# Kernel tuning notes

Hardware: AMD Instinct MI355X
Metric: run time of the kernel (lower is better)

## Reference

```python
import jax, jax.numpy as jnp
import numpy as np

DIM, NH, NS = 384, 8, 3
HID = int(DIM * 4.0)
R1 = max(1, int(min(DIM, HID) * 0.5))   # 192
R2 = max(1, int(min(HID, DIM) * 0.5))   # 192
SPLIT = DIM // NS                        # 128
HD = DIM // NH                           # 48


def _ln(x, g, b, eps=1e-6):
    m = jnp.mean(x, axis=-1, keepdims=True)
    v = jnp.mean(jnp.square(x - m), axis=-1, keepdims=True)
    return (x - m) * jax.lax.rsqrt(v + eps) * g + b


def _dwconv(x, w, b):
    # x: [B, SPLIT, H, W]; w: [SPLIT, 1, 3, 3] depthwise (groups=SPLIT)
    y = jax.lax.conv_general_dilated(
        x, w, window_strides=(1, 1), padding='SAME',
        dimension_numbers=('NCHW', 'OIHW', 'NCHW'),
        feature_group_count=SPLIT)
    return y + b[None, :, None, None]


def setup_inputs() -> dict:
    key = jax.random.key(0)
    ks = jax.random.split(key, 16)
    s = lambda *sh: 0.02
    inp = {
        'x': jax.random.normal(ks[0], (16, DIM, 56, 56), jnp.float32),
        'dw_w0': jax.random.normal(ks[1], (SPLIT, 1, 3, 3), jnp.float32) * 0.1,
        'dw_b0': jnp.zeros((SPLIT,), jnp.float32),
        'dw_w1': jax.random.normal(ks[2], (SPLIT, 1, 3, 3), jnp.float32) * 0.1,
        'dw_b1': jnp.zeros((SPLIT,), jnp.float32),
        'ln1_g': jnp.ones((DIM,), jnp.float32),
        'ln1_b': jnp.zeros((DIM,), jnp.float32),
        'qkv_w': jax.random.normal(ks[3], (DIM, 3 * DIM), jnp.float32) * 0.02,
        'proj_w': jax.random.normal(ks[4], (DIM, DIM), jnp.float32) * 0.02,
        'proj_b': jnp.zeros((DIM,), jnp.float32),
        'ln2_g': jnp.ones((DIM,), jnp.float32),
        'ln2_b': jnp.zeros((DIM,), jnp.float32),
        'mlp1_dw': jax.random.normal(ks[5], (DIM, R1), jnp.float32) * 0.02,
        'mlp1_uw': jax.random.normal(ks[6], (R1, HID), jnp.float32) * 0.02,
        'mlp1_ub': jnp.zeros((HID,), jnp.float32),
        'mlp2_dw': jax.random.normal(ks[7], (HID, R2), jnp.float32) * 0.02,
        'mlp2_uw': jax.random.normal(ks[8], (R2, DIM), jnp.float32) * 0.02,
        'mlp2_ub': jnp.zeros((DIM,), jnp.float32),
    }
    return inp


def reference(x, dw_w0, dw_b0, dw_w1, dw_b1, ln1_g, ln1_b, qkv_w,
              proj_w, proj_b, ln2_g, ln2_b,
              mlp1_dw, mlp1_uw, mlp1_ub, mlp2_dw, mlp2_uw, mlp2_ub):
    B, C, H, W = x.shape
    # multi-scale depthwise residual chain
    s0, s1, s2 = jnp.split(x, NS, axis=1)
    s1 = _dwconv(s1 + s0, dw_w0, dw_b0)
    s2 = _dwconv(s2 + s1, dw_w1, dw_b1)
    x = jnp.concatenate([s0, s1, s2], axis=1)

    N = H * W
    x_flat = jnp.transpose(x.reshape(B, C, N), (0, 2, 1))  # [B, N, C]
    y = _ln(x_flat, ln1_g, ln1_b)
    qkv = (y @ qkv_w).reshape(B, N, 3, NH, HD)
    q = jnp.transpose(qkv[:, :, 0], (0, 2, 3, 1))  # [B, NH, HD, N]
    k = jnp.transpose(qkv[:, :, 1], (0, 2, 3, 1))
    v = jnp.transpose(qkv[:, :, 2], (0, 2, 3, 1))
    # L2 normalize over token dim (XCA)
    q = q / jnp.maximum(jnp.linalg.norm(q, axis=-1, keepdims=True), 1e-12)
    k = k / jnp.maximum(jnp.linalg.norm(k, axis=-1, keepdims=True), 1e-12)
    attn = jnp.einsum('bhdn,bhen->bhde', q, k)  # [B, NH, HD, HD]
    attn = jax.nn.softmax(attn, axis=-1)
    y = jnp.einsum('bhde,bhen->bhdn', attn, v)  # [B, NH, HD, N]
    y = jnp.transpose(y, (0, 3, 1, 2)).reshape(B, N, C)
    y = y @ proj_w + proj_b
    x_flat = x_flat + y

    z = _ln(x_flat, ln2_g, ln2_b)
    h = jax.nn.gelu((z @ mlp1_dw) @ mlp1_uw + mlp1_ub, approximate=False)
    z = (h @ mlp2_dw) @ mlp2_uw + mlp2_ub
    x_flat = x_flat + z
    return jnp.transpose(x_flat, (0, 2, 1)).reshape(B, C, H, W)
```

## Files before the change

kernel.cpp:

```cpp
#include <hip/hip_runtime.h>


typedef __attribute__((ext_vector_type(8))) short short8;
typedef __attribute__((ext_vector_type(4))) float floatx4;

#define NB 16
#define DIM 384
#define NTOK 3136
#define TTOK 50176
#define NH 8
#define HD 48

__device__ __forceinline__ unsigned short f2bf(float f) {
  union { float f; unsigned int u; } v; v.f = f;
  unsigned int u = v.u;
  unsigned int r = (u + 0x7FFFu + ((u >> 16) & 1u)) >> 16;
  return (unsigned short)r;
}
__device__ __forceinline__ float bf2f(unsigned short h) {
  union { unsigned int u; float f; } v; v.u = ((unsigned int)h) << 16;
  return v.f;
}

__device__ __forceinline__ void gload_lds16(const unsigned short* g, unsigned short* l) {
  __builtin_amdgcn_global_load_lds(
      (const __attribute__((address_space(1))) unsigned int*)g,
      (__attribute__((address_space(3))) unsigned int*)l, 16, 0, 0);
}

__global__ void wtrans(const float* __restrict__ w, unsigned short* __restrict__ wt,
                       int K, int N) {
  int g = blockIdx.x * 256 + threadIdx.x;
  if (g < K * N) {
    int k = g / N, n = g % N;
    wt[(size_t)n * K + k] = f2bf(w[g]);
  }
}

__global__ void dwconv(const float* __restrict__ a, long bsA,
                       const float* __restrict__ b2, long bsB,
                       const float* __restrict__ w, const float* __restrict__ bias,
                       float* __restrict__ dst) {
  int g = blockIdx.x * 256 + threadIdx.x;
  int xx = g % 56;
  int yy = (g / 56) % 56;
  int c  = (g / NTOK) % 128;
  int b  = g / (NTOK * 128);
  const float* pa = a  + (size_t)b * bsA + (size_t)c * NTOK;
  const float* pb = b2 + (size_t)b * bsB + (size_t)c * NTOK;
  float acc = bias[c];
  #pragma unroll
  for (int ky = 0; ky < 3; ky++) {
    int y2 = yy + ky - 1;
    if (y2 < 0 || y2 >= 56) continue;
    #pragma unroll
    for (int kx = 0; kx < 3; kx++) {
      int x2 = xx + kx - 1;
      if (x2 < 0 || x2 >= 56) continue;
      acc += w[c * 9 + ky * 3 + kx] * (pa[y2 * 56 + x2] + pb[y2 * 56 + x2]);
    }
  }
  dst[((size_t)b * 128 + c) * NTOK + yy * 56 + xx] = acc;
}

__global__ __launch_bounds__(256) void build_ln1(
    const float* __restrict__ x, const float* __restrict__ s1,
    const float* __restrict__ s2, const float* __restrict__ g,
    const float* __restrict__ bb, float* __restrict__ xflat,
    unsigned short* __restrict__ y, unsigned short* __restrict__ yT) {
  __shared__ float tile[384 * 33];
  __shared__ float psum[8][32], psumsq[8][32];
  __shared__ float smean[32], srs[32];
  int blk = blockIdx.x;
  int b = blk / 98, n0 = (blk % 98) * 32;
  int t = threadIdx.x;
  int nl = t & 31, crow = t >> 5;

  #pragma unroll 4
  for (int i = 0; i < 48; i++) {
    int c = i * 8 + crow;
    float v;
    if (c < 128)      v = x[((size_t)b * DIM + c) * NTOK + n0 + nl];
    else if (c < 256) v = s1[((size_t)b * 128 + (c - 128)) * NTOK + n0 + nl];
    else              v = s2[((size_t)b * 128 + (c - 256)) * NTOK + n0 + nl];
    tile[c * 33 + nl] = v;
  }
  __syncthreads();

  {
    int seg = t >> 5, tok = t & 31;
    float s = 0.f, sq = 0.f;
    #pragma unroll 8
    for (int cc = 0; cc < 48; cc++) {
      float v = tile[(seg * 48 + cc) * 33 + tok];
      s += v; sq += v * v;
    }
    psum[seg][tok] = s; psumsq[seg][tok] = sq;
  }
  __syncthreads();
  if (t < 32) {
    float s = 0.f, sq = 0.f;
    #pragma unroll
    for (int seg = 0; seg < 8; seg++) { s += psum[seg][t]; sq += psumsq[seg][t]; }
    float mean = s * (1.f / DIM);
    float var = sq * (1.f / DIM) - mean * mean;
    smean[t] = mean;
    srs[t] = rsqrtf(var + 1e-6f);
  }
  __syncthreads();

  #pragma unroll 4
  for (int i = 0; i < 48; i++) {
    int idx = i * 256 + t;
    int tok = idx / 384, c = idx - tok * 384;
    float v = tile[c * 33 + tok];
    float vn = (v - smean[tok]) * srs[tok] * g[c] + bb[c];
    size_t o = (size_t)(b * NTOK + n0 + tok) * DIM + c;
    xflat[o] = v;
    y[o] = f2bf(vn);
    tile[c * 33 + tok] = vn;
  }
  __syncthreads();
  #pragma unroll 4
  for (int i = 0; i < 48; i++) {
    int idx = i * 256 + t;
    int c = idx >> 5, tok = idx & 31;
    yT[((size_t)b * DIM + c) * NTOK + n0 + tok] = f2bf(tile[c * 33 + tok]);
  }
}

__global__ __launch_bounds__(256) void ln_rows(
    const float* __restrict__ in, const float* __restrict__ g,
    const float* __restrict__ bb, unsigned short* __restrict__ out) {
  int tkn = blockIdx.x * 4 + (threadIdx.x >> 6);
  int lane = threadIdx.x & 63;
  const float* row = in + (size_t)tkn * DIM;
  float v[6];
  float s = 0.f, sq = 0.f;
  #pragma unroll
  for (int i = 0; i < 6; i++) {
    int c = lane + i * 64;
    v[i] = row[c]; s += v[i]; sq += v[i] * v[i];
  }
  #pragma unroll
  for (int off = 32; off; off >>= 1) {
    s += __shfl_xor(s, off);
    sq += __shfl_xor(sq, off);
  }
  float mean = s * (1.f / DIM);
  float var = sq * (1.f / DIM) - mean * mean;
  float rs = rsqrtf(var + 1e-6f);
  #pragma unroll
  for (int i = 0; i < 6; i++) {
    int c = lane + i * 64;
    out[(size_t)tkn * DIM + c] = f2bf((v[i] - mean) * rs * g[c] + bb[c]);
  }
}

template<int BN, int MODE>
__global__ __launch_bounds__(256) void gemmx(
    const unsigned short* __restrict__ A, const unsigned short* __restrict__ Bt,
    const float* __restrict__ bias, const float* __restrict__ resid,
    void* __restrict__ out, int M, int N, int K, int lda, int ldb,
    int nsplit, long aBatch, long aSplit, long bBatch, long bSplit, long cBatch) {
  constexpr int MT = (BN == 128) ? 4 : 2;
  constexpr int NT = 4;
  __shared__ __align__(16) unsigned short As[128 * 32];
  __shared__ __align__(16) unsigned short Bs[BN * 32];
  const int tid = threadIdx.x;
  const int w = tid >> 6, lane = tid & 63;
  const int quad = lane >> 4, r16 = lane & 15;

  const int nwg = gridDim.x * gridDim.y;
  const int bid = blockIdx.y * gridDim.x + blockIdx.x;
  const int q8 = nwg >> 3, r8 = nwg & 7;
  const int xcd = bid & 7, loc = bid >> 3;
  const int swz = (xcd < r8 ? xcd * (q8 + 1) : r8 * (q8 + 1) + (xcd - r8) * q8) + loc;
  const int bx = swz % gridDim.x, by = swz / gridDim.x;
  const int row0 = by * 128, col0 = bx * BN;

  const int z = blockIdx.z;
  const int bz = z / nsplit, sz = z - bz * nsplit;
  A  += bz * aBatch + sz * aSplit;
  Bt += bz * bBatch + sz * bSplit;
  const size_t cOff = (size_t)z * cBatch;

  const int wm = (BN == 128) ? (w >> 1) * 64 : w * 32;
  const int wn = (BN == 128) ? (w & 1) * 64 : 0;
  const int lrow = lane >> 2;
  const int lcol = (lane & 3) * 8;

  const unsigned short* aP0 = A + (size_t)(row0 + w * 32 + lrow) * lda + lcol;
  const unsigned short* aP1 = aP0 + (size_t)16 * lda;
  const unsigned short* bP0 = Bt + (size_t)(col0 + ((BN == 128) ? w * 32 : w * 16) + lrow) * ldb + lcol;
  const unsigned short* bP1 = bP0 + (size_t)16 * ldb;

  floatx4 acc[MT][NT] = {};

  for (int k0 = 0; k0 < K; k0 += 32) {
    gload_lds16(aP0 + k0, &As[(2 * w) * 512]);
    gload_lds16(aP1 + k0, &As[(2 * w + 1) * 512]);
    if (BN == 128) {
      gload_lds16(bP0 + k0, &Bs[(2 * w) * 512]);
      gload_lds16(bP1 + k0, &Bs[(2 * w + 1) * 512]);
    } else {
      gload_lds16(bP0 + k0, &Bs[w * 512]);
    }
    __syncthreads();
    short8 af[MT], bfr[NT];
    #pragma unroll
    for (int mi = 0; mi < MT; mi++)
      af[mi] = *(const short8*)(&As[(wm + mi * 16 + r16) * 32 + quad * 8]);
    #pragma unroll
    for (int ni = 0; ni < NT; ni++)
      bfr[ni] = *(const short8*)(&Bs[(wn + ni * 16 + r16) * 32 + quad * 8]);
    #pragma unroll
    for (int mi = 0; mi < MT; mi++)
      #pragma unroll
      for (int ni = 0; ni < NT; ni++)
        acc[mi][ni] = __builtin_amdgcn_mfma_f32_16x16x32_bf16(af[mi], bfr[ni], acc[mi][ni], 0, 0, 0);
    __syncthreads();
  }

  #pragma unroll
  for (int mi = 0; mi < MT; mi++)
    #pragma unroll
    for (int ni = 0; ni < NT; ni++)
      #pragma unroll
      for (int p = 0; p < 4; p++) {
        int row = row0 + wm + mi * 16 + quad * 4 + p;
        int col = col0 + wn + ni * 16 + r16;
        size_t idx = (size_t)row * N + col;
        float v = acc[mi][ni][p];
        if (MODE == 0) {
          ((unsigned short*)out)[cOff + idx] = f2bf(v);
        } else if (MODE == 1) {
          v += bias[col];
          v = 0.5f * v * (1.0f + erff(v * 0.70710678118654752f));
          ((unsigned short*)out)[idx] = f2bf(v);
        } else if (MODE == 2) {
          v += bias[col] + resid[idx];
          ((float*)out)[idx] = v;
        } else {
          ((float*)out)[cOff + idx] = v;
        }
      }
}

__global__ __launch_bounds__(256) void gsum(const unsigned short* __restrict__ Gp,
                                            unsigned short* __restrict__ Gbf) {
  int b = blockIdx.x / 576;
  int i = (blockIdx.x % 576) * 256 + threadIdx.x;
  float s = 0.f;
  #pragma unroll
  for (int p = 0; p < 7; p++)
    s += bf2f(Gp[((size_t)(b * 7 + p)) * 147456 + i]);
  Gbf[(size_t)b * 147456 + i] = f2bf(s);
}

__global__ __launch_bounds__(256) void attn_finish2(
    const float* __restrict__ P, const unsigned short* __restrict__ qkvT,
    const float* __restrict__ qkv_w, float* __restrict__ attnb) {
  __shared__ unsigned short wkT[48 * 392];
  __shared__ float Ss[48 * 49];
  __shared__ float qn[48], kn[48];
  int bh = blockIdx.x, b = bh >> 3, h = bh & 7;
  int t = threadIdx.x;
  const float* Pb = P + (size_t)b * 294912;

  #pragma unroll
  for (int i = 0; i < 9; i++) {
    int idx = t + i * 256;
    int e = idx / 48, j = idx - e * 48;
    *(short8*)(&wkT[e * 392 + j * 8]) =
        *(const short8*)(&qkvT[(size_t)(384 + h * 48 + e) * 384 + j * 8]);
  }
  if (t < 48) {
    const float* pr = Pb + (size_t)(h * 48 + t) * 384;
    const float* wc = qkv_w + h * 48 + t;
    float s = 0.f;
    #pragma unroll 8
    for (int c = 0; c < 384; c++) s += pr[c] * wc[(size_t)c * 1152];
    qn[t] = fmaxf(sqrtf(fmaxf(s, 0.f)), 1e-12f);
  } else if (t >= 64 && t < 112) {
    int e = t - 64;
    const float* pr = Pb + (size_t)(384 + h * 48 + e) * 384;
    const float* wc = qkv_w + 384 + h * 48 + e;
    float s = 0.f;
    #pragma unroll 8
    for (int c = 0; c < 384; c++) s += pr[c] * wc[(size_t)c * 1152];
    kn[e] = fmaxf(sqrtf(fmaxf(s, 0.f)), 1e-12f);
  }
  __syncthreads();

  int d0 = (t >> 4) * 3, e0 = (t & 15) * 3;
  float acc[3][3] = {};
  const float* pq0 = Pb + (size_t)(h * 48 + d0) * 384;
  for (int c8 = 0; c8 < 48; c8++) {
    floatx4 pv[3][2];
    #pragma unroll
    for (int i = 0; i < 3; i++) {
      pv[i][0] = *(const floatx4*)(pq0 + (size_t)i * 384 + c8 * 8);
      pv[i][1] = *(const floatx4*)(pq0 + (size_t)i * 384 + c8 * 8 + 4);
    }
    #pragma unroll
    for (int j = 0; j < 3; j++) {
      short8 wv = *(const short8*)(&wkT[(e0 + j) * 392 + c8 * 8]);
      #pragma unroll
      for (int kk = 0; kk < 4; kk++) {
        float wa = bf2f((unsigned short)wv[kk]);
        float wb = bf2f((unsigned short)wv[4 + kk]);
        #pragma unroll
        for (int i = 0; i < 3; i++)
          acc[i][j] += pv[i][0][kk] * wa + pv[i][1][kk] * wb;
      }
    }
  }
  #pragma unroll
  for (int i = 0; i < 3; i++)
    #pragma unroll
    for (int j = 0; j < 3; j++)
      Ss[(d0 + i) * 49 + e0 + j] = acc[i][j] / (qn[d0 + i] * kn[e0 + j]);
  __syncthreads();

  if (t < 48) {
    float m = -1e30f;
    for (int e = 0; e < 48; e++) m = fmaxf(m, Ss[t * 49 + e]);
    float ssum = 0.f;
    float ex[48];
    for (int e = 0; e < 48; e++) { ex[e] = expf(Ss[t * 49 + e] - m); ssum += ex[e]; }
    float inv = 1.f / ssum;
    float* op = attnb + (size_t)bh * 2304 + t * 48;
    for (int e = 0; e < 48; e++) op[e] = ex[e] * inv;
  }
}

__global__ __launch_bounds__(256) void attn_apply(
    const unsigned short* __restrict__ vbf, const float* __restrict__ attnb,
    unsigned short* __restrict__ yat) {
  __shared__ float at[48 * 52];
  __shared__ float vs[64 * 56];
  int bh = blockIdx.x / 49, chunk = blockIdx.x % 49;
  int b = bh >> 3, h = bh & 7;
  int t = threadIdx.x;
  int lane = t & 63, w = t >> 6;
  #pragma unroll
  for (int i = 0; i < 9; i++) {
    int idx = t + i * 256;
    if (idx < 2304) at[(idx / 48) * 52 + idx % 48] = attnb[(size_t)bh * 2304 + idx];
  }
  #pragma unroll
  for (int i = 0; i < 2; i++) {
    int idx = t + i * 256;
    if (idx < 384) {
      int r = idx / 6, j = idx - r * 6;
      short8 vv = *(const short8*)(&vbf[((size_t)b * NTOK + chunk * 64 + r) * 384
                                        + h * HD + j * 8]);
      floatx4 f0, f1;
      #pragma unroll
      for (int kk = 0; kk < 4; kk++) {
        f0[kk] = bf2f((unsigned short)vv[kk]);
        f1[kk] = bf2f((unsigned short)vv[4 + kk]);
      }
      *(floatx4*)(&vs[r * 56 + j * 8]) = f0;
      *(floatx4*)(&vs[r * 56 + j * 8 + 4]) = f1;
    }
  }
  __syncthreads();
  floatx4 v4[12];
  #pragma unroll
  for (int j = 0; j < 12; j++)
    v4[j] = *(const floatx4*)(&vs[lane * 56 + j * 4]);
  float r[12];
  #pragma unroll
  for (int dd = 0; dd < 12; dd++) {
    int d = w * 12 + dd;
    floatx4 a = {};
    #pragma unroll
    for (int j = 0; j < 12; j++)
      a += *(const floatx4*)(&at[d * 52 + j * 4]) * v4[j];
    r[dd] = a[0] + a[1] + a[2] + a[3];
  }
  size_t wo = ((size_t)b * NTOK + chunk * 64 + lane) * DIM + h * HD + w * 12;
  unsigned int* op = (unsigned int*)(yat + wo);
  #pragma unroll
  for (int j = 0; j < 6; j++)
    op[j] = (unsigned int)f2bf(r[2 * j]) | ((unsigned int)f2bf(r[2 * j + 1]) << 16);
}

__global__ __launch_bounds__(256) void transpose_out(const float* __restrict__ in,
                                                     float* __restrict__ out) {
  __shared__ float tile[32][33];
  int b = blockIdx.z, ct = blockIdx.y, nt = blockIdx.x;
  int t = threadIdx.x;
  int cc = t & 31, rr = t >> 5;
  #pragma unroll
  for (int i = 0; i < 4; i++) {
    int nn = rr + i * 8;
    tile[nn][cc] = in[((size_t)b * NTOK + nt * 32 + nn) * DIM + ct * 32 + cc];
  }
  __syncthreads();
  #pragma unroll
  for (int i = 0; i < 4; i++) {
    int c2 = rr + i * 8;
    out[((size_t)b * DIM + ct * 32 + c2) * NTOK + nt * 32 + cc] = tile[cc][c2];
  }
}

extern "C" void kernel_launch(void* const* d_in, const int* in_sizes, int n_in,
                              void* d_out, int out_size, void* d_ws, size_t ws_size,
                              hipStream_t stream) {
  const float* x       = (const float*)d_in[0];
  const float* dw_w0   = (const float*)d_in[1];
  const float* dw_b0   = (const float*)d_in[2];
  const float* dw_w1   = (const float*)d_in[3];
  const float* dw_b1   = (const float*)d_in[4];
  const float* ln1_g   = (const float*)d_in[5];
  const float* ln1_b   = (const float*)d_in[6];
  const float* qkv_w   = (const float*)d_in[7];
  const float* proj_w  = (const float*)d_in[8];
  const float* proj_b  = (const float*)d_in[9];
  const float* ln2_g   = (const float*)d_in[10];
  const float* ln2_b   = (const float*)d_in[11];
  const float* mlp1_dw = (const float*)d_in[12];
  const float* mlp1_uw = (const float*)d_in[13];
  const float* mlp1_ub = (const float*)d_in[14];
  const float* mlp2_dw = (const float*)d_in[15];
  const float* mlp2_uw = (const float*)d_in[16];
  const float* mlp2_ub = (const float*)d_in[17];
  float* out = (float*)d_out;
  char* ws = (char*)d_ws;

  float*          xflat = (float*)(ws + 0);
  float*          s1ws  = (float*)(ws + 77070336);
  float*          s2ws  = (float*)(ws + 102760448);
  unsigned short* vbf   = (unsigned short*)(ws + 77070336);
  unsigned short* ybf   = (unsigned short*)(ws + 128450560);
  unsigned short* ybfT  = (unsigned short*)(ws + 166985728);
  unsigned short* G_part= (unsigned short*)(ws + 128450560);
  unsigned short* Gbf   = (unsigned short*)(ws + 205520896);
  float*          P     = (float*)(ws + 210239488);
  unsigned short* yat   = (unsigned short*)(ws + 166985728);
  float*          xres  = (float*)(ws + 77070336);
  unsigned short* zbf   = (unsigned short*)(ws + 0);
  unsigned short* h1    = (unsigned short*)(ws + 38535168);
  unsigned short* h3    = (unsigned short*)(ws + 57802752);
  unsigned short* h2    = (unsigned short*)(ws + 154140672);
  unsigned short* qkvT  = (unsigned short*)(ws + 231211008);
  unsigned short* projT = (unsigned short*)(ws + 232095744);
  unsigned short* m1dT  = (unsigned short*)(ws + 232390656);
  unsigned short* m1uT  = (unsigned short*)(ws + 232538112);
  unsigned short* m2dT  = (unsigned short*)(ws + 233127936);
  unsigned short* m2uT  = (unsigned short*)(ws + 233717760);
  float*          attnb = (float*)(ws + 233914368);

  wtrans<<<1728, 256, 0, stream>>>(qkv_w, qkvT, 384, 1152);
  wtrans<<<576, 256, 0, stream>>>(proj_w, projT, 384, 384);
  wtrans<<<288, 256, 0, stream>>>(mlp1_dw, m1dT, 384, 192);
  wtrans<<<1152, 256, 0, stream>>>(mlp1_uw, m1uT, 192, 1536);
  wtrans<<<1152, 256, 0, stream>>>(mlp2_dw, m2dT, 1536, 192);
  wtrans<<<288, 256, 0, stream>>>(mlp2_uw, m2uT, 192, 384);

  dwconv<<<25088, 256, 0, stream>>>(x + 128 * NTOK, (long)DIM * NTOK,
                                    x, (long)DIM * NTOK, dw_w0, dw_b0, s1ws);
  dwconv<<<25088, 256, 0, stream>>>(x + 256 * NTOK, (long)DIM * NTOK,
                                    s1ws, (long)128 * NTOK, dw_w1, dw_b1, s2ws);

  build_ln1<<<1568, 256, 0, stream>>>(x, s1ws, s2ws, ln1_g, ln1_b, xflat, ybf, ybfT);

  gemmx<128, 0><<<dim3(3, 392), 256, 0, stream>>>(
      ybf, qkvT + 768 * 384, nullptr, nullptr, vbf,
      TTOK, 384, 384, 384, 384, 1, 0, 0, 0, 0, 0);

  gemmx<128, 0><<<dim3(3, 3, 112), 256, 0, stream>>>(
      ybfT, ybfT, nullptr, nullptr, G_part,
      384, 384, 448, 3136, 3136, 7,
      (long)384 * 3136, 448L, (long)384 * 3136, 448L, 147456L);
  gsum<<<9216, 256, 0, stream>>>(G_part, Gbf);

  gemmx<128, 3><<<dim3(3, 6, 16), 256, 0, stream>>>(
      qkvT, Gbf, nullptr, nullptr, P,
      768, 384, 384, 384, 384, 1,
      0, 0, 147456L, 0, 294912L);
  attn_finish2<<<NB * NH, 256, 0, stream>>>(P, qkvT, qkv_w, attnb);

  attn_apply<<<NB * NH * 49, 256, 0, stream>>>(vbf, attnb, yat);

  gemmx<128, 2><<<dim3(3, 392), 256, 0, stream>>>(
      yat, projT, proj_b, xflat, xres,
      TTOK, 384, 384, 384, 384, 1, 0, 0, 0, 0, 0);
  ln_rows<<<12544, 256, 0, stream>>>(xres, ln2_g, ln2_b, zbf);
  gemmx<64, 0><<<dim3(3, 392), 256, 0, stream>>>(
      zbf, m1dT, nullptr, nullptr, h1,
      TTOK, 192, 384, 384, 384, 1, 0, 0, 0, 0, 0);
  for (int half = 0; half < 2; half++) {
    const unsigned short* h1p = h1 + (size_t)half * 25088 * 192;
    unsigned short* h3p = h3 + (size_t)half * 25088 * 192;
    gemmx<128, 1><<<dim3(12, 196), 256, 0, stream>>>(
        h1p, m1uT, mlp1_ub, nullptr, h2,
        25088, 1536, 192, 192, 192, 1, 0, 0, 0, 0, 0);
    gemmx<64, 0><<<dim3(3, 196), 256, 0, stream>>>(
        h2, m2dT, nullptr, nullptr, h3p,
        25088, 192, 1536, 1536, 1536, 1, 0, 0, 0, 0, 0);
  }
  gemmx<128, 2><<<dim3(3, 392), 256, 0, stream>>>(
      h3, m2uT, mlp2_ub, xres, xres,
      TTOK, 384, 192, 192, 192, 1, 0, 0, 0, 0, 0);
  transpose_out<<<dim3(98, 12, 16), 256, 0, stream>>>(xres, out);
}
```

Baseline: 816.9 us.

## Fuse MLP up-projection, GELU and down-projection into one kernel

Replaces the two-GEMM sequence (h1→h2 with GELU, then h2→h3), which wrote a large 1536-wide bf16 intermediate to global memory, with one fused kernel. Each block keeps 64 rows of h1 in LDS, computes 128-column chunks of the hidden activation, applies bias and GELU into an LDS tile, and accumulates the down-projection in registers. This removes the global round trip of the hidden tensor. The cost is that weights are read straight from global or cache without LDS staging, and with only 784 blocks of 64-row tiles per-block compute efficiency and occupancy may be worse than the tuned GEMM.

```diff
diff --git a/kernel.cpp b/kernel.cpp
--- a/kernel.cpp
+++ b/kernel.cpp
@@ -244,6 +244,89 @@
         } else {
           ((float*)out)[cOff + idx] = v;
         }
+      }
+}
+
+__global__ __launch_bounds__(256) void mlp_mid(
+    const unsigned short* __restrict__ h1, const unsigned short* __restrict__ m1uT,
+    const unsigned short* __restrict__ m2dT, const float* __restrict__ bias,
+    unsigned short* __restrict__ h3) {
+  __shared__ __align__(16) unsigned short h1s[64 * 200];
+  __shared__ __align__(16) unsigned short ts[64 * 136];
+  const int t = threadIdx.x;
+  const int w = t >> 6, lane = t & 63;
+  const int quad = lane >> 4, r16 = lane & 15;
+  const int row0 = blockIdx.x * 64;
+
+  #pragma unroll
+  for (int i = 0; i < 6; i++) {
+    int c = t + i * 256;
+    int r = c / 24, off = (c - r * 24) * 8;
+    *(short8*)(&h1s[r * 200 + off]) =
+        *(const short8*)(&h1[(size_t)(row0 + r) * 192 + off]);
+  }
+  __syncthreads();
+
+  floatx4 acc2[4][3] = {};
+  for (int j = 0; j < 12; j++) {
+    floatx4 acc1[4][2] = {};
+    #pragma unroll
+    for (int kk = 0; kk < 6; kk++) {
+      short8 af[4], bf[2];
+      #pragma unroll
+      for (int mi = 0; mi < 4; mi++)
+        af[mi] = *(const short8*)(&h1s[(mi * 16 + r16) * 200 + kk * 32 + quad * 8]);
+      #pragma unroll
+      for (int ni = 0; ni < 2; ni++)
+        bf[ni] = *(const short8*)(&m1uT[(size_t)(j * 128 + w * 32 + ni * 16 + r16) * 192
+                                        + kk * 32 + quad * 8]);
+      #pragma unroll
+      for (int mi = 0; mi < 4; mi++)
+        #pragma unroll
+        for (int ni = 0; ni < 2; ni++)
+          acc1[mi][ni] = __builtin_amdgcn_mfma_f32_16x16x32_bf16(af[mi], bf[ni], acc1[mi][ni], 0, 0, 0);
+    }
+    __syncthreads();
+    #pragma unroll
+    for (int mi = 0; mi < 4; mi++)
+      #pragma unroll
+      for (int ni = 0; ni < 2; ni++) {
+        int col = w * 32 + ni * 16 + r16;
+        float bv = bias[j * 128 + col];
+        #pragma unroll
+        for (int p = 0; p < 4; p++) {
+          float v = acc1[mi][ni][p] + bv;
+          v = 0.5f * v * (1.0f + erff(v * 0.70710678118654752f));
+          ts[(mi * 16 + quad * 4 + p) * 136 + col] = f2bf(v);
+        }
+      }
+    __syncthreads();
+    #pragma unroll
+    for (int kk = 0; kk < 4; kk++) {
+      short8 af2[4], bf2[3];
+      #pragma unroll
+      for (int mi = 0; mi < 4; mi++)
+        af2[mi] = *(const short8*)(&ts[(mi * 16 + r16) * 136 + kk * 32 + quad * 8]);
+      #pragma unroll
+      for (int ni = 0; ni < 3; ni++)
+        bf2[ni] = *(const short8*)(&m2dT[(size_t)(w * 48 + ni * 16 + r16) * 1536
+                                         + j * 128 + kk * 32 + quad * 8]);
+      #pragma unroll
+      for (int mi = 0; mi < 4; mi++)
+        #pragma unroll
+        for (int ni = 0; ni < 3; ni++)
+          acc2[mi][ni] = __builtin_amdgcn_mfma_f32_16x16x32_bf16(af2[mi], bf2[ni], acc2[mi][ni], 0, 0, 0);
+    }
+  }
+  #pragma unroll
+  for (int mi = 0; mi < 4; mi++)
+    #pragma unroll
+    for (int ni = 0; ni < 3; ni++)
+      #pragma unroll
+      for (int p = 0; p < 4; p++) {
+        int row = row0 + mi * 16 + quad * 4 + p;
+        int col = w * 48 + ni * 16 + r16;
+        h3[(size_t)row * 192 + col] = f2bf(acc2[mi][ni][p]);
       }
 }
 
@@ -445,7 +528,6 @@
   unsigned short* zbf   = (unsigned short*)(ws + 0);
   unsigned short* h1    = (unsigned short*)(ws + 38535168);
   unsigned short* h3    = (unsigned short*)(ws + 57802752);
-  unsigned short* h2    = (unsigned short*)(ws + 154140672);
   unsigned short* qkvT  = (unsigned short*)(ws + 231211008);
   unsigned short* projT = (unsigned short*)(ws + 232095744);
   unsigned short* m1dT  = (unsigned short*)(ws + 232390656);
@@ -493,16 +575,7 @@
   gemmx<64, 0><<<dim3(3, 392), 256, 0, stream>>>(
       zbf, m1dT, nullptr, nullptr, h1,
       TTOK, 192, 384, 384, 384, 1, 0, 0, 0, 0, 0);
-  for (int half = 0; half < 2; half++) {
-    const unsigned short* h1p = h1 + (size_t)half * 25088 * 192;
-    unsigned short* h3p = h3 + (size_t)half * 25088 * 192;
-    gemmx<128, 1><<<dim3(12, 196), 256, 0, stream>>>(
-        h1p, m1uT, mlp1_ub, nullptr, h2,
-        25088, 1536, 192, 192, 192, 1, 0, 0, 0, 0, 0);
-    gemmx<64, 0><<<dim3(3, 196), 256, 0, stream>>>(
-        h2, m2dT, nullptr, nullptr, h3p,
-        25088, 192, 1536, 1536, 1536, 1, 0, 0, 0, 0, 0);
-  }
+  mlp_mid<<<784, 256, 0, stream>>>(h1, m1uT, m2dT, mlp1_ub, h3);
   gemmx<128, 2><<<dim3(3, 392), 256, 0, stream>>>(
       h3, m2uT, mlp2_ub, xres, xres,
       TTOK, 384, 192, 192, 192, 1, 0, 0, 0, 0, 0);
```

Result: slower. 852.4 us (+4.3%).

## Double-buffer LDS tiles in gemm to overlap global loads with MFMA

Applied to the files above, without the earlier changes.

The GEMM kernel now keeps two LDS buffers for the A and B tiles and prefetches the next K-slice with direct global-to-LDS loads while the current slice is consumed. Explicit vmcnt waits replace the full __syncthreads so that only the current tile's loads are waited on. This aims to hide global memory latency behind the matrix-core work, at the cost of doubled LDS use and fragile hand-counted waitcnt values. Occupancy may drop because of the extra shared memory.

```diff
diff --git a/kernel.cpp b/kernel.cpp
--- a/kernel.cpp
+++ b/kernel.cpp
@@ -165,8 +165,8 @@
     int nsplit, long aBatch, long aSplit, long bBatch, long bSplit, long cBatch) {
   constexpr int MT = (BN == 128) ? 4 : 2;
   constexpr int NT = 4;
-  __shared__ __align__(16) unsigned short As[128 * 32];
-  __shared__ __align__(16) unsigned short Bs[BN * 32];
+  __shared__ __align__(16) unsigned short As[2][128 * 32];
+  __shared__ __align__(16) unsigned short Bs[2][BN * 32];
   const int tid = threadIdx.x;
   const int w = tid >> 6, lane = tid & 63;
   const int quad = lane >> 4, r16 = lane & 15;
@@ -195,31 +195,53 @@
   const unsigned short* bP0 = Bt + (size_t)(col0 + ((BN == 128) ? w * 32 : w * 16) + lrow) * ldb + lcol;
   const unsigned short* bP1 = bP0 + (size_t)16 * ldb;
 
+  const int nk = K >> 5;
+
+  gload_lds16(aP0, &As[0][(2 * w) * 512]);
+  gload_lds16(aP1, &As[0][(2 * w + 1) * 512]);
+  if (BN == 128) {
+    gload_lds16(bP0, &Bs[0][(2 * w) * 512]);
+    gload_lds16(bP1, &Bs[0][(2 * w + 1) * 512]);
+  } else {
+    gload_lds16(bP0, &Bs[0][w * 512]);
+  }
+
   floatx4 acc[MT][NT] = {};
 
-  for (int k0 = 0; k0 < K; k0 += 32) {
-    gload_lds16(aP0 + k0, &As[(2 * w) * 512]);
-    gload_lds16(aP1 + k0, &As[(2 * w + 1) * 512]);
-    if (BN == 128) {
-      gload_lds16(bP0 + k0, &Bs[(2 * w) * 512]);
-      gload_lds16(bP1 + k0, &Bs[(2 * w + 1) * 512]);
+  for (int ki = 0; ki < nk; ki++) {
+    const int cur = ki & 1;
+    if (ki + 1 < nk) {
+      const int kn = (ki + 1) * 32;
+      gload_lds16(aP0 + kn, &As[cur ^ 1][(2 * w) * 512]);
+      gload_lds16(aP1 + kn, &As[cur ^ 1][(2 * w + 1) * 512]);
+      if (BN == 128) {
+        gload_lds16(bP0 + kn, &Bs[cur ^ 1][(2 * w) * 512]);
+        gload_lds16(bP1 + kn, &Bs[cur ^ 1][(2 * w + 1) * 512]);
+      } else {
+        gload_lds16(bP0 + kn, &Bs[cur ^ 1][w * 512]);
+      }
+      if (BN == 128) asm volatile("s_waitcnt vmcnt(4)" ::: "memory");
+      else           asm volatile("s_waitcnt vmcnt(3)" ::: "memory");
     } else {
-      gload_lds16(bP0 + k0, &Bs[w * 512]);
+      asm volatile("s_waitcnt vmcnt(0)" ::: "memory");
     }
-    __syncthreads();
+    __builtin_amdgcn_s_barrier();
+
     short8 af[MT], bfr[NT];
     #pragma unroll
     for (int mi = 0; mi < MT; mi++)
-      af[mi] = *(const short8*)(&As[(wm + mi * 16 + r16) * 32 + quad * 8]);
+      af[mi] = *(const short8*)(&As[cur][(wm + mi * 16 + r16) * 32 + quad * 8]);
     #pragma unroll
     for (int ni = 0; ni < NT; ni++)
-      bfr[ni] = *(const short8*)(&Bs[(wn + ni * 16 + r16) * 32 + quad * 8]);
+      bfr[ni] = *(const short8*)(&Bs[cur][(wn + ni * 16 + r16) * 32 + quad * 8]);
     #pragma unroll
     for (int mi = 0; mi < MT; mi++)
       #pragma unroll
       for (int ni = 0; ni < NT; ni++)
         acc[mi][ni] = __builtin_amdgcn_mfma_f32_16x16x32_bf16(af[mi], bfr[ni], acc[mi][ni], 0, 0, 0);
-    __syncthreads();
+
+    asm volatile("s_waitcnt lgkmcnt(0)" ::: "memory");
+    __builtin_amdgcn_s_barrier();
   }
 
   #pragma unroll
```

Result: slower. 847.8 us (+3.8%).

## Store residual stream in bf16 and fuse output transpose into final GEMM epilogue

Applied to the files above, without the earlier changes.

The intermediate residual after the attention projection is now written as bf16 instead of fp32, which halves its write and its two later reads (LN2 and the final residual add). The final MLP GEMM gets a new epilogue mode that adds bias and the bf16 residual, then writes straight into the NCHW output with 4-float vector stores. This removes the separate transpose_out kernel and its full fp32 round trip. In exchange the residual loses precision, and the transposed stores are strided across channels.

```diff
diff --git a/kernel.cpp b/kernel.cpp
--- a/kernel.cpp
+++ b/kernel.cpp
@@ -130,17 +130,17 @@
 }
 
 __global__ __launch_bounds__(256) void ln_rows(
-    const float* __restrict__ in, const float* __restrict__ g,
+    const unsigned short* __restrict__ in, const float* __restrict__ g,
     const float* __restrict__ bb, unsigned short* __restrict__ out) {
   int tkn = blockIdx.x * 4 + (threadIdx.x >> 6);
   int lane = threadIdx.x & 63;
-  const float* row = in + (size_t)tkn * DIM;
+  const unsigned short* row = in + (size_t)tkn * DIM;
   float v[6];
   float s = 0.f, sq = 0.f;
   #pragma unroll
   for (int i = 0; i < 6; i++) {
     int c = lane + i * 64;
-    v[i] = row[c]; s += v[i]; sq += v[i] * v[i];
+    v[i] = bf2f(row[c]); s += v[i]; sq += v[i] * v[i];
   }
   #pragma unroll
   for (int off = 32; off; off >>= 1) {
@@ -160,7 +160,7 @@
 template<int BN, int MODE>
 __global__ __launch_bounds__(256) void gemmx(
     const unsigned short* __restrict__ A, const unsigned short* __restrict__ Bt,
-    const float* __restrict__ bias, const float* __restrict__ resid,
+    const float* __restrict__ bias, const void* __restrict__ resid,
     void* __restrict__ out, int M, int N, int K, int lda, int ldb,
     int nsplit, long aBatch, long aSplit, long bBatch, long bSplit, long cBatch) {
   constexpr int MT = (BN == 128) ? 4 : 2;
@@ -225,26 +225,39 @@
   #pragma unroll
   for (int mi = 0; mi < MT; mi++)
     #pragma unroll
-    for (int ni = 0; ni < NT; ni++)
-      #pragma unroll
-      for (int p = 0; p < 4; p++) {
-        int row = row0 + wm + mi * 16 + quad * 4 + p;
+    for (int ni = 0; ni < NT; ni++) {
+      if (MODE == 4) {
+        int r0 = row0 + wm + mi * 16 + quad * 4;
         int col = col0 + wn + ni * 16 + r16;
-        size_t idx = (size_t)row * N + col;
-        float v = acc[mi][ni][p];
-        if (MODE == 0) {
-          ((unsigned short*)out)[cOff + idx] = f2bf(v);
-        } else if (MODE == 1) {
-          v += bias[col];
-          v = 0.5f * v * (1.0f + erff(v * 0.70710678118654752f));
-          ((unsigned short*)out)[idx] = f2bf(v);
-        } else if (MODE == 2) {
-          v += bias[col] + resid[idx];
-          ((float*)out)[idx] = v;
-        } else {
-          ((float*)out)[cOff + idx] = v;
+        int bq = r0 / NTOK, nn = r0 - bq * NTOK;
+        floatx4 vv;
+        #pragma unroll
+        for (int p = 0; p < 4; p++)
+          vv[p] = acc[mi][ni][p] + bias[col] +
+                  bf2f(((const unsigned short*)resid)[(size_t)(r0 + p) * N + col]);
+        *(floatx4*)&((float*)out)[((size_t)bq * DIM + col) * NTOK + nn] = vv;
+      } else {
+        #pragma unroll
+        for (int p = 0; p < 4; p++) {
+          int row = row0 + wm + mi * 16 + quad * 4 + p;
+          int col = col0 + wn + ni * 16 + r16;
+          size_t idx = (size_t)row * N + col;
+          float v = acc[mi][ni][p];
+          if (MODE == 0) {
+            ((unsigned short*)out)[cOff + idx] = f2bf(v);
+          } else if (MODE == 1) {
+            v += bias[col];
+            v = 0.5f * v * (1.0f + erff(v * 0.70710678118654752f));
+            ((unsigned short*)out)[idx] = f2bf(v);
+          } else if (MODE == 2) {
+            v += bias[col] + ((const float*)resid)[idx];
+            ((unsigned short*)out)[idx] = f2bf(v);
+          } else {
+            ((float*)out)[cOff + idx] = v;
+          }
         }
       }
+    }
 }
 
 __global__ __launch_bounds__(256) void gsum(const unsigned short* __restrict__ Gp,
@@ -386,25 +399,6 @@
   #pragma unroll
   for (int j = 0; j < 6; j++)
     op[j] = (unsigned int)f2bf(r[2 * j]) | ((unsigned int)f2bf(r[2 * j + 1]) << 16);
-}
-
-__global__ __launch_bounds__(256) void transpose_out(const float* __restrict__ in,
-                                                     float* __restrict__ out) {
-  __shared__ float tile[32][33];
-  int b = blockIdx.z, ct = blockIdx.y, nt = blockIdx.x;
-  int t = threadIdx.x;
-  int cc = t & 31, rr = t >> 5;
-  #pragma unroll
-  for (int i = 0; i < 4; i++) {
-    int nn = rr + i * 8;
-    tile[nn][cc] = in[((size_t)b * NTOK + nt * 32 + nn) * DIM + ct * 32 + cc];
-  }
-  __syncthreads();
-  #pragma unroll
-  for (int i = 0; i < 4; i++) {
-    int c2 = rr + i * 8;
-    out[((size_t)b * DIM + ct * 32 + c2) * NTOK + nt * 32 + cc] = tile[cc][c2];
-  }
 }
 
 extern "C" void kernel_launch(void* const* d_in, const int* in_sizes, int n_in,
@@ -441,7 +435,7 @@
   unsigned short* Gbf   = (unsigned short*)(ws + 205520896);
   float*          P     = (float*)(ws + 210239488);
   unsigned short* yat   = (unsigned short*)(ws + 166985728);
-  float*          xres  = (float*)(ws + 77070336);
+  unsigned short* xres  = (unsigned short*)(ws + 77070336);
   unsigned short* zbf   = (unsigned short*)(ws + 0);
   unsigned short* h1    = (unsigned short*)(ws + 38535168);
   unsigned short* h3    = (unsigned short*)(ws + 57802752);
@@ -503,8 +497,7 @@
         h2, m2dT, nullptr, nullptr, h3p,
         25088, 192, 1536, 1536, 1536, 1, 0, 0, 0, 0, 0);
   }
-  gemmx<128, 2><<<dim3(3, 392), 256, 0, stream>>>(
-      h3, m2uT, mlp2_ub, xres, xres,
+  gemmx<128, 4><<<dim3(3, 392), 256, 0, stream>>>(
+      h3, m2uT, mlp2_ub, xres, out,
       TTOK, 384, 192, 192, 192, 1, 0, 0, 0, 0, 0);
-  transpose_out<<<dim3(98, 12, 16), 256, 0, stream>>>(xres, out);
-}
+}
```

New measurement: 797.4 us. -2.4%, faster.
